# Kernel tuning notes

Measured on AMD Instinct MI355X. Metric: run time of the kernel, lower is better.

The kernel has to match this reference:

```python
import jax, jax.numpy as jnp
import numpy as np

B, T, D = 8, 1024, 1024

def setup_inputs() -> dict:
    key = jax.random.key(0)
    ks = jax.random.split(key, 9)
    s = D ** -0.5
    return {
        "x": jax.random.normal(ks[0], (B, T, D), dtype=jnp.float32),
        "w_q": jax.random.normal(ks[1], (D, D), dtype=jnp.float32) * s,
        "b_q": jax.random.normal(ks[2], (D,), dtype=jnp.float32) * 0.02,
        "w_k": jax.random.normal(ks[3], (D, D), dtype=jnp.float32) * s,
        "b_k": jax.random.normal(ks[4], (D,), dtype=jnp.float32) * 0.02,
        "w_v": jax.random.normal(ks[5], (D, D), dtype=jnp.float32) * s,
        "b_v": jax.random.normal(ks[6], (D,), dtype=jnp.float32) * 0.02,
        "w_o": jax.random.normal(ks[7], (D, D), dtype=jnp.float32) * s,
        "b_o": jax.random.normal(ks[8], (D,), dtype=jnp.float32) * 0.02,
    }

def reference(x, w_q, b_q, w_k, b_k, w_v, b_v, w_o, b_o):
    d = x.shape[-1]
    scale = jnp.asarray(d, x.dtype) ** -0.5
    q = jnp.einsum('btd,ed->bte', x, w_q) + b_q  # nn.Linear: x @ W^T + b
    k = jnp.einsum('btd,ed->bte', x, w_k) + b_k
    v = jnp.einsum('btd,ed->bte', x, w_v) + b_v
    t = x.shape[1]
    causal = jnp.tril(jnp.ones((t, t), dtype=bool))  # (T, T)
    scores = jnp.einsum('bqd,bkd->bqk', q, k) * scale
    scores = jnp.where(causal, scores, -jnp.inf)
    attn = jax.nn.softmax(scores, axis=-1)  # max-subtraction folded in
    out = jnp.einsum('bqk,bkd->bqd', attn, v)
    return jnp.einsum('btd,ed->bte', out, w_o) + b_o
```

## Files before the change

### kernel.cpp

```cpp
#include <hip/hip_runtime.h>

typedef unsigned short u16;
typedef __attribute__((ext_vector_type(8))) short short8;
typedef __attribute__((ext_vector_type(4))) float f32x4;


__device__ __forceinline__ u16 f2bf(float f) {
  unsigned u = __builtin_bit_cast(unsigned, f);
  u += 0x7fffu + ((u >> 16) & 1u);
  return (u16)(u >> 16);
}

__device__ __forceinline__ void gload16(const void* g, void* l) {
  __builtin_amdgcn_global_load_lds(
      (const __attribute__((address_space(1))) unsigned*)g,
      (__attribute__((address_space(3))) unsigned*)l, 16, 0, 0);
}

__device__ __forceinline__ void gemm_tile(
    const u16* __restrict__ A, int lda,
    const u16* __restrict__ B, int ldb,
    int m0, int n0, int kend,
    char* sA, char* sB, f32x4 acc[4][4])
{
  const int tid  = threadIdx.x;
  const int lane = tid & 63;
  const int wave = tid >> 6;
  const int quad = lane >> 4;
  const int l16  = lane & 15;
  const int wr   = (wave >> 1) << 6;
  const int wc   = (wave & 1) << 6;

  const u16* ga[4]; const u16* gb[4]; int lb[4];
#pragma unroll
  for (int j = 0; j < 4; ++j) {
    const int Lb = j * 256 + wave * 64;
    const int L  = Lb + lane;
    const int r  = L >> 3;
    const int c  = (L & 7) ^ (r & 7);
    lb[j] = Lb * 16;
    ga[j] = A + (size_t)(m0 + r) * lda + c * 8;
    gb[j] = B + (size_t)(n0 + r) * ldb + c * 8;
  }

  for (int kt = 0; kt < kend; kt += 64) {
#pragma unroll
    for (int j = 0; j < 4; ++j) {
      gload16(ga[j], sA + lb[j]);
      gload16(gb[j], sB + lb[j]);
      ga[j] += 64; gb[j] += 64;
    }
    __syncthreads();
#pragma unroll
    for (int kk = 0; kk < 2; ++kk) {
      short8 af[4], bfr[4];
#pragma unroll
      for (int i = 0; i < 4; ++i) {
        const int rm = wr + i * 16 + l16;
        af[i]  = *(const short8*)(sA + rm * 128 + (((kk << 2) + quad) ^ (rm & 7)) * 16);
        const int rn = wc + i * 16 + l16;
        bfr[i] = *(const short8*)(sB + rn * 128 + (((kk << 2) + quad) ^ (rn & 7)) * 16);
      }
#pragma unroll
      for (int i = 0; i < 4; ++i)
#pragma unroll
        for (int j = 0; j < 4; ++j)
          acc[i][j] = __builtin_amdgcn_mfma_f32_16x16x32_bf16(af[i], bfr[j], acc[i][j], 0, 0, 0);
    }
    __syncthreads();
  }
}

__device__ __forceinline__ void gemm_tile_64(
    const u16* __restrict__ A, int lda,
    const u16* __restrict__ B, int ldb,
    int m0, int n0, int kend,
    char* sA, char* sB, f32x4 acc[2][4])
{
  const int tid  = threadIdx.x;
  const int lane = tid & 63;
  const int wave = tid >> 6;
  const int quad = lane >> 4;
  const int l16  = lane & 15;
  const int wr   = (wave >> 1) << 5;
  const int wc   = (wave & 1) << 6;

  const u16* ga[2]; int la[2];
  const u16* gb[4]; int lb[4];
#pragma unroll
  for (int j = 0; j < 2; ++j) {
    const int Lb = j * 256 + wave * 64;
    const int L  = Lb + lane;
    const int r  = L >> 3;
    const int c  = (L & 7) ^ (r & 7);
    la[j] = Lb * 16;
    ga[j] = A + (size_t)(m0 + r) * lda + c * 8;
  }
#pragma unroll
  for (int j = 0; j < 4; ++j) {
    const int Lb = j * 256 + wave * 64;
    const int L  = Lb + lane;
    const int r  = L >> 3;
    const int c  = (L & 7) ^ (r & 7);
    lb[j] = Lb * 16;
    gb[j] = B + (size_t)(n0 + r) * ldb + c * 8;
  }

  for (int kt = 0; kt < kend; kt += 64) {
#pragma unroll
    for (int j = 0; j < 2; ++j) { gload16(ga[j], sA + la[j]); ga[j] += 64; }
#pragma unroll
    for (int j = 0; j < 4; ++j) { gload16(gb[j], sB + lb[j]); gb[j] += 64; }
    __syncthreads();
#pragma unroll
    for (int kk = 0; kk < 2; ++kk) {
      short8 af[2], bfr[4];
#pragma unroll
      for (int i = 0; i < 2; ++i) {
        const int rm = wr + i * 16 + l16;
        af[i] = *(const short8*)(sA + rm * 128 + (((kk << 2) + quad) ^ (rm & 7)) * 16);
      }
#pragma unroll
      for (int j = 0; j < 4; ++j) {
        const int rn = wc + j * 16 + l16;
        bfr[j] = *(const short8*)(sB + rn * 128 + (((kk << 2) + quad) ^ (rn & 7)) * 16);
      }
#pragma unroll
      for (int i = 0; i < 2; ++i)
#pragma unroll
        for (int j = 0; j < 4; ++j)
          acc[i][j] = __builtin_amdgcn_mfma_f32_16x16x32_bf16(af[i], bfr[j], acc[i][j], 0, 0, 0);
    }
    __syncthreads();
  }
}

#define ACC_ZERO4(acc) { _Pragma("unroll") for (int i=0;i<4;++i) \
  _Pragma("unroll") for (int j=0;j<4;++j) \
  _Pragma("unroll") for (int r=0;r<4;++r) acc[i][j][r]=0.f; }
#define ACC_ZERO2(acc) { _Pragma("unroll") for (int i=0;i<2;++i) \
  _Pragma("unroll") for (int j=0;j<4;++j) \
  _Pragma("unroll") for (int r=0;r<4;++r) acc[i][j][r]=0.f; }

__device__ __forceinline__ void store_tile_bf16(
    f32x4 acc[4][4], const float* bias, int nbias0,
    u16* C, int m0, int n0, int ldc, char* smem)
{
  const int tid = threadIdx.x, lane = tid & 63, wave = tid >> 6;
  const int quad = lane >> 4, l16 = lane & 15;
  const int wr = (wave >> 1) << 6, wc = (wave & 1) << 6;
  u16* t = (u16*)smem;
#pragma unroll
  for (int j = 0; j < 4; ++j) {
    const int nn = wc + j * 16 + l16;
    const float bj = bias ? bias[nbias0 + nn] : 0.f;
#pragma unroll
    for (int i = 0; i < 4; ++i) {
      const int mm = wr + i * 16 + quad * 4;
#pragma unroll
      for (int r = 0; r < 4; ++r)
        t[(mm + r) * 136 + nn] = f2bf(acc[i][j][r] + bj);
    }
  }
  __syncthreads();
#pragma unroll
  for (int it = 0; it < 8; ++it) {
    const int L = it * 256 + tid;
    const int mm = L >> 4, cc = L & 15;
    *(uint4*)(C + (size_t)(m0 + mm) * ldc + n0 + cc * 8) =
        *(const uint4*)(t + mm * 136 + cc * 8);
  }
}

__global__ __launch_bounds__(256) void cast_inputs(
    const float* __restrict__ x,  const float* __restrict__ wq,
    const float* __restrict__ wk, const float* __restrict__ wv,
    const float* __restrict__ wo,
    u16* xb, u16* wqb, u16* wkb, u16* wvb, u16* wob, float* rsum)
{
  int b = blockIdx.x;
  if (b < 8) {
    float4 z = {0.f, 0.f, 0.f, 0.f};
    *(float4*)(rsum + (b * 256 + threadIdx.x) * 4) = z;
  }
  const float* src; u16* dst; int base;
  if (b < 4096) { src = x; dst = xb; base = b * 2048; }
  else {
    int r = (b - 4096) >> 9, bb = (b - 4096) & 511;
    base = bb * 2048;
    src = (r == 0) ? wq : (r == 1) ? wk : (r == 2) ? wv : wo;
    dst = (r == 0) ? wqb : (r == 1) ? wkb : (r == 2) ? wvb : wob;
  }
  int i0 = base + threadIdx.x * 8;
  float4 f0 = *(const float4*)(src + i0);
  float4 f1 = *(const float4*)(src + i0 + 4);
  short8 o;
  o[0]=(short)f2bf(f0.x); o[1]=(short)f2bf(f0.y); o[2]=(short)f2bf(f0.z); o[3]=(short)f2bf(f0.w);
  o[4]=(short)f2bf(f1.x); o[5]=(short)f2bf(f1.y); o[6]=(short)f2bf(f1.z); o[7]=(short)f2bf(f1.w);
  *(short8*)(dst + i0) = o;
}

__global__ __launch_bounds__(256) void proj_qkv(
    const u16* __restrict__ xb,
    const u16* __restrict__ wqb, const u16* __restrict__ wkb, const u16* __restrict__ wvb,
    const float* __restrict__ bq, const float* __restrict__ bk, const float* __restrict__ bv,
    u16* q, u16* k, u16* vt)
{
  __shared__ char smem[34816];
  char* sA = smem; char* sB = smem + 16384;
  const int z = blockIdx.z;
  const u16* W = (z == 0) ? wqb : (z == 1) ? wkb : wvb;
  const float* bias = (z == 0) ? bq : (z == 1) ? bk : bv;
  const int id = blockIdx.x + 8 * blockIdx.y;
  const int m0 = ((id & 7) * 8 + (id >> 6)) * 128;
  const int n0 = ((id >> 3) & 7) * 128;

  f32x4 acc[4][4]; ACC_ZERO4(acc);
  gemm_tile(xb, 1024, W, 1024, m0, n0, 1024, sA, sB, acc);

  if (z < 2) {
    store_tile_bf16(acc, bias, n0, (z == 0) ? q : k, m0, n0, 1024, smem);
  } else {
    const int tid = threadIdx.x, lane = tid & 63, wave = tid >> 6;
    const int quad = lane >> 4, l16 = lane & 15;
    const int wr = (wave >> 1) << 6, wc = (wave & 1) << 6;
    u16* t = (u16*)smem;
#pragma unroll
    for (int j = 0; j < 4; ++j) {
      const int nn = wc + j * 16 + l16;
      const float bj = bias[n0 + nn];
#pragma unroll
      for (int i = 0; i < 4; ++i) {
        const int mm = wr + i * 16 + quad * 4;
#pragma unroll
        for (int r = 0; r < 4; ++r)
          t[nn * 136 + mm + r] = f2bf(acc[i][j][r] + bj);
      }
    }
    __syncthreads();
    const int b = m0 >> 10, t0 = m0 & 1023;
#pragma unroll
    for (int it = 0; it < 8; ++it) {
      const int L = it * 256 + tid;
      const int nn = L >> 4, cc = L & 15;
      *(uint4*)(vt + ((size_t)b << 20) + (size_t)(n0 + nn) * 1024 + t0 + cc * 8) =
          *(const uint4*)(t + nn * 136 + cc * 8);
    }
  }
}

__global__ __launch_bounds__(256) void qk_expscores(
    const u16* __restrict__ q, const u16* __restrict__ k,
    u16* __restrict__ probs, float* __restrict__ rowsum)
{
  const int id = blockIdx.x;
  const int b = id / 72, t = id - b * 72;
  int p = (int)((__builtin_sqrtf((float)(4 * t + 1)) - 1.f) * 0.5f);
  while ((p + 1) * (p + 2) <= t) ++p;
  while (p * (p + 1) > t) --p;
  int r0 = t - p * (p + 1);
  const int qi = 2 * p + (r0 >= p + 1);
  const int kb = (r0 >= p + 1) ? r0 - (p + 1) : r0;

  __shared__ char smem[24576];
  char* sA = smem; char* sB = smem + 8192;
  const u16* A = q + ((size_t)b << 20);
  const u16* B = k + ((size_t)b << 20);
  const int m0 = qi * 64, n0 = kb * 128;

  f32x4 acc[2][4]; ACC_ZERO2(acc);
  gemm_tile_64(A, 1024, B, 1024, m0, n0, 1024, sA, sB, acc);

  const int tid = threadIdx.x, lane = tid & 63, wave = tid >> 6;
  const int quad = lane >> 4, l16 = lane & 15;
  const int wr = (wave >> 1) << 5, wc = (wave & 1) << 6;
  const bool diag = (kb == (qi >> 1));

  float part[2][4];
#pragma unroll
  for (int i = 0; i < 2; ++i)
#pragma unroll
    for (int r = 0; r < 4; ++r) part[i][r] = 0.f;

  u16* tl = (u16*)smem;
#pragma unroll
  for (int j = 0; j < 4; ++j) {
    const int nn = wc + j * 16 + l16;
#pragma unroll
    for (int i = 0; i < 2; ++i) {
      const int mm = wr + i * 16 + quad * 4;
#pragma unroll
      for (int r = 0; r < 4; ++r) {
        float e = __expf(acc[i][j][r] * 0.03125f);
        if (diag && (n0 + nn) > (m0 + mm + r)) e = 0.f;
        part[i][r] += e;
        tl[(mm + r) * 136 + nn] = f2bf(e);
      }
    }
  }
  float* rs = rowsum + b * 1024 + m0;
#pragma unroll
  for (int i = 0; i < 2; ++i)
#pragma unroll
    for (int r = 0; r < 4; ++r) {
      float v = part[i][r];
      v += __shfl_xor(v, 1); v += __shfl_xor(v, 2);
      v += __shfl_xor(v, 4); v += __shfl_xor(v, 8);
      if (l16 == 0) atomicAdd(rs + wr + i * 16 + quad * 4 + r, v);
    }
  __syncthreads();
  u16* C = probs + ((size_t)b << 20);
#pragma unroll
  for (int it = 0; it < 4; ++it) {
    const int L = it * 256 + tid;
    const int mm = L >> 4, cc = L & 15;
    *(uint4*)(C + (size_t)(m0 + mm) * 1024 + n0 + cc * 8) =
        *(const uint4*)(tl + mm * 136 + cc * 8);
  }
}

__global__ __launch_bounds__(256) void pv_gemm(
    const u16* __restrict__ probs, const u16* __restrict__ vt,
    const float* __restrict__ rowsum, u16* __restrict__ o)
{
  const int id = blockIdx.x;
  const int b = id & 7, nb = (id >> 3) & 7, qi = 15 - (id >> 6);
  __shared__ char smem[24576];
  char* sA = smem; char* sB = smem + 8192;
  const u16* A = probs + ((size_t)b << 20);
  const u16* B = vt + ((size_t)b << 20);
  const int m0 = qi * 64, n0 = nb * 128;
  const int kend = (qi + 1) * 64;

  f32x4 acc[2][4]; ACC_ZERO2(acc);
  gemm_tile_64(A, 1024, B, 1024, m0, n0, kend, sA, sB, acc);

  const int tid = threadIdx.x, lane = tid & 63, wave = tid >> 6;
  const int quad = lane >> 4, l16 = lane & 15;
  const int wr = (wave >> 1) << 5, wc = (wave & 1) << 6;
  const float* rs = rowsum + b * 1024 + m0;
  u16* tl = (u16*)smem;
#pragma unroll
  for (int i = 0; i < 2; ++i)
#pragma unroll
    for (int r = 0; r < 4; ++r) {
      const int mm = wr + i * 16 + quad * 4 + r;
      const float inv = 1.0f / rs[mm];
#pragma unroll
      for (int j = 0; j < 4; ++j)
        tl[mm * 136 + wc + j * 16 + l16] = f2bf(acc[i][j][r] * inv);
    }
  __syncthreads();
  u16* C = o + ((size_t)b << 20);
#pragma unroll
  for (int it = 0; it < 4; ++it) {
    const int L = it * 256 + tid;
    const int mm = L >> 4, cc = L & 15;
    *(uint4*)(C + (size_t)(m0 + mm) * 1024 + n0 + cc * 8) =
        *(const uint4*)(tl + mm * 136 + cc * 8);
  }
}

__global__ __launch_bounds__(256) void proj_o(
    const u16* __restrict__ ob, const u16* __restrict__ wob,
    const float* __restrict__ bo, float* __restrict__ out)
{
  __shared__ char smem[34816];
  char* sA = smem; char* sB = smem + 8192;
  const int id = blockIdx.x;
  const int m0 = ((id & 7) * 16 + (id >> 6)) * 64;
  const int n0 = ((id >> 3) & 7) * 128;
  f32x4 acc[2][4]; ACC_ZERO2(acc);
  gemm_tile_64(ob, 1024, wob, 1024, m0, n0, 1024, sA, sB, acc);

  const int tid = threadIdx.x, lane = tid & 63, wave = tid >> 6;
  const int quad = lane >> 4, l16 = lane & 15;
  const int wr = (wave >> 1) << 5, wc = (wave & 1) << 6;
  float* tf = (float*)smem;
#pragma unroll
  for (int j = 0; j < 4; ++j) {
    const int nn = wc + j * 16 + l16;
    const float bj = bo[n0 + nn];
#pragma unroll
    for (int i = 0; i < 2; ++i)
#pragma unroll
      for (int r = 0; r < 4; ++r)
        tf[(wr + i * 16 + quad * 4 + r) * 132 + nn] = acc[i][j][r] + bj;
  }
  __syncthreads();
#pragma unroll
  for (int it = 0; it < 8; ++it) {
    const int L = it * 256 + tid;
    const int mm = L >> 5, cc = L & 31;
    *(float4*)(out + (size_t)(m0 + mm) * 1024 + n0 + cc * 4) =
        *(const float4*)(tf + mm * 132 + cc * 4);
  }
}

extern "C" void kernel_launch(void* const* d_in, const int* in_sizes, int n_in,
                              void* d_out, int out_size, void* d_ws, size_t ws_size,
                              hipStream_t stream) {
  const float* x  = (const float*)d_in[0];
  const float* wq = (const float*)d_in[1];
  const float* bq = (const float*)d_in[2];
  const float* wk = (const float*)d_in[3];
  const float* bk = (const float*)d_in[4];
  const float* wv = (const float*)d_in[5];
  const float* bv = (const float*)d_in[6];
  const float* wo = (const float*)d_in[7];
  const float* bo = (const float*)d_in[8];
  float* out = (float*)d_out;

  char* ws = (char*)d_ws;
  const size_t MB = 1u << 20;
  u16*  xb  = (u16*)(ws);
  u16*  wqb = (u16*)(ws + 16*MB);
  u16*  wkb = (u16*)(ws + 18*MB);
  u16*  wvb = (u16*)(ws + 20*MB);
  u16*  wob = (u16*)(ws + 22*MB);
  u16*  qb  = (u16*)(ws + 24*MB);
  u16*  kb  = (u16*)(ws + 40*MB);
  u16*  vtb = (u16*)(ws + 56*MB);
  u16*  pr  = (u16*)(ws + 72*MB);
  float* rsum = (float*)(ws + 88*MB);

  cast_inputs<<<6144, 256, 0, stream>>>(x, wq, wk, wv, wo, xb, wqb, wkb, wvb, wob, rsum);
  proj_qkv<<<dim3(8, 64, 3), 256, 0, stream>>>(xb, wqb, wkb, wvb, bq, bk, bv, qb, kb, vtb);
  qk_expscores<<<576, 256, 0, stream>>>(qb, kb, pr, rsum);
  pv_gemm<<<1024, 256, 0, stream>>>(pr, vtb, rsum, xb );
  proj_o<<<1024, 256, 0, stream>>>(xb, wob, bo, out);
}
```

Measured before the change: 225.8 us.

## Fuse Q and K projections to share the X tile across two weight tiles

Splits the combined QKV projection into a fused Q+K kernel and a separate V kernel. The Q+K kernel loads each X tile into LDS once and multiplies it against both the W_q and W_k tiles, keeping two 64-float accumulator sets per thread. This removes one of the redundant X tile loads and halves the X traffic for Q and K. In exchange it doubles accumulator register pressure (lower occupancy), uses more LDS, and adds a second kernel launch for V.

```diff
diff --git a/kernel.cpp b/kernel.cpp
--- a/kernel.cpp
+++ b/kernel.cpp
@@ -200,52 +200,112 @@
   *(short8*)(dst + i0) = o;
 }
 
-__global__ __launch_bounds__(256) void proj_qkv(
+__global__ __launch_bounds__(256) void proj_qk(
     const u16* __restrict__ xb,
-    const u16* __restrict__ wqb, const u16* __restrict__ wkb, const u16* __restrict__ wvb,
-    const float* __restrict__ bq, const float* __restrict__ bk, const float* __restrict__ bv,
-    u16* q, u16* k, u16* vt)
+    const u16* __restrict__ wqb, const u16* __restrict__ wkb,
+    const float* __restrict__ bq, const float* __restrict__ bk,
+    u16* q, u16* k)
+{
+  __shared__ char smem[49152];
+  char* sA = smem; char* sQ = smem + 16384; char* sK = smem + 32768;
+  const int id = blockIdx.x;
+  const int m0 = ((id & 7) * 8 + (id >> 6)) * 128;
+  const int n0 = ((id >> 3) & 7) * 128;
+
+  const int tid = threadIdx.x, lane = tid & 63, wave = tid >> 6;
+  const int quad = lane >> 4, l16 = lane & 15;
+  const int wr = (wave >> 1) << 6, wc = (wave & 1) << 6;
+
+  const u16* ga[4]; const u16* gq[4]; const u16* gk[4]; int lb[4];
+#pragma unroll
+  for (int j = 0; j < 4; ++j) {
+    const int Lb = j * 256 + wave * 64;
+    const int L  = Lb + lane;
+    const int r  = L >> 3;
+    const int c  = (L & 7) ^ (r & 7);
+    lb[j] = Lb * 16;
+    ga[j] = xb  + (size_t)(m0 + r) * 1024 + c * 8;
+    gq[j] = wqb + (size_t)(n0 + r) * 1024 + c * 8;
+    gk[j] = wkb + (size_t)(n0 + r) * 1024 + c * 8;
+  }
+
+  f32x4 accQ[4][4], accK[4][4];
+  ACC_ZERO4(accQ); ACC_ZERO4(accK);
+
+  for (int kt = 0; kt < 1024; kt += 64) {
+#pragma unroll
+    for (int j = 0; j < 4; ++j) {
+      gload16(ga[j], sA + lb[j]);
+      gload16(gq[j], sQ + lb[j]);
+      gload16(gk[j], sK + lb[j]);
+      ga[j] += 64; gq[j] += 64; gk[j] += 64;
+    }
+    __syncthreads();
+#pragma unroll
+    for (int kk = 0; kk < 2; ++kk) {
+      short8 af[4], bqf[4], bkf[4];
+#pragma unroll
+      for (int i = 0; i < 4; ++i) {
+        const int rm = wr + i * 16 + l16;
+        const int rn = wc + i * 16 + l16;
+        const int co = (kk << 2) + quad;
+        af[i]  = *(const short8*)(sA + rm * 128 + ((co ^ (rm & 7)) * 16));
+        bqf[i] = *(const short8*)(sQ + rn * 128 + ((co ^ (rn & 7)) * 16));
+        bkf[i] = *(const short8*)(sK + rn * 128 + ((co ^ (rn & 7)) * 16));
+      }
+#pragma unroll
+      for (int i = 0; i < 4; ++i)
+#pragma unroll
+        for (int j = 0; j < 4; ++j) {
+          accQ[i][j] = __builtin_amdgcn_mfma_f32_16x16x32_bf16(af[i], bqf[j], accQ[i][j], 0, 0, 0);
+          accK[i][j] = __builtin_amdgcn_mfma_f32_16x16x32_bf16(af[i], bkf[j], accK[i][j], 0, 0, 0);
+        }
+    }
+    __syncthreads();
+  }
+
+  store_tile_bf16(accQ, bq, n0, q, m0, n0, 1024, smem);
+  __syncthreads();
+  store_tile_bf16(accK, bk, n0, k, m0, n0, 1024, smem);
+}
+
+__global__ __launch_bounds__(256) void proj_v(
+    const u16* __restrict__ xb, const u16* __restrict__ wvb,
+    const float* __restrict__ bv, u16* vt)
 {
   __shared__ char smem[34816];
   char* sA = smem; char* sB = smem + 16384;
-  const int z = blockIdx.z;
-  const u16* W = (z == 0) ? wqb : (z == 1) ? wkb : wvb;
-  const float* bias = (z == 0) ? bq : (z == 1) ? bk : bv;
-  const int id = blockIdx.x + 8 * blockIdx.y;
+  const int id = blockIdx.x;
   const int m0 = ((id & 7) * 8 + (id >> 6)) * 128;
   const int n0 = ((id >> 3) & 7) * 128;
 
   f32x4 acc[4][4]; ACC_ZERO4(acc);
-  gemm_tile(xb, 1024, W, 1024, m0, n0, 1024, sA, sB, acc);
-
-  if (z < 2) {
-    store_tile_bf16(acc, bias, n0, (z == 0) ? q : k, m0, n0, 1024, smem);
-  } else {
-    const int tid = threadIdx.x, lane = tid & 63, wave = tid >> 6;
-    const int quad = lane >> 4, l16 = lane & 15;
-    const int wr = (wave >> 1) << 6, wc = (wave & 1) << 6;
-    u16* t = (u16*)smem;
-#pragma unroll
-    for (int j = 0; j < 4; ++j) {
-      const int nn = wc + j * 16 + l16;
-      const float bj = bias[n0 + nn];
-#pragma unroll
-      for (int i = 0; i < 4; ++i) {
-        const int mm = wr + i * 16 + quad * 4;
-#pragma unroll
-        for (int r = 0; r < 4; ++r)
-          t[nn * 136 + mm + r] = f2bf(acc[i][j][r] + bj);
-      }
-    }
-    __syncthreads();
-    const int b = m0 >> 10, t0 = m0 & 1023;
-#pragma unroll
-    for (int it = 0; it < 8; ++it) {
-      const int L = it * 256 + tid;
-      const int nn = L >> 4, cc = L & 15;
-      *(uint4*)(vt + ((size_t)b << 20) + (size_t)(n0 + nn) * 1024 + t0 + cc * 8) =
-          *(const uint4*)(t + nn * 136 + cc * 8);
-    }
+  gemm_tile(xb, 1024, wvb, 1024, m0, n0, 1024, sA, sB, acc);
+
+  const int tid = threadIdx.x, lane = tid & 63, wave = tid >> 6;
+  const int quad = lane >> 4, l16 = lane & 15;
+  const int wr = (wave >> 1) << 6, wc = (wave & 1) << 6;
+  u16* t = (u16*)smem;
+#pragma unroll
+  for (int j = 0; j < 4; ++j) {
+    const int nn = wc + j * 16 + l16;
+    const float bj = bv[n0 + nn];
+#pragma unroll
+    for (int i = 0; i < 4; ++i) {
+      const int mm = wr + i * 16 + quad * 4;
+#pragma unroll
+      for (int r = 0; r < 4; ++r)
+        t[nn * 136 + mm + r] = f2bf(acc[i][j][r] + bj);
+    }
+  }
+  __syncthreads();
+  const int b = m0 >> 10, t0 = m0 & 1023;
+#pragma unroll
+  for (int it = 0; it < 8; ++it) {
+    const int L = it * 256 + tid;
+    const int nn = L >> 4, cc = L & 15;
+    *(uint4*)(vt + ((size_t)b << 20) + (size_t)(n0 + nn) * 1024 + t0 + cc * 8) =
+        *(const uint4*)(t + nn * 136 + cc * 8);
   }
 }
 
@@ -425,7 +485,8 @@
   float* rsum = (float*)(ws + 88*MB);
 
   cast_inputs<<<6144, 256, 0, stream>>>(x, wq, wk, wv, wo, xb, wqb, wkb, wvb, wob, rsum);
-  proj_qkv<<<dim3(8, 64, 3), 256, 0, stream>>>(xb, wqb, wkb, wvb, bq, bk, bv, qb, kb, vtb);
+  proj_qk<<<512, 256, 0, stream>>>(xb, wqb, wkb, bq, bk, qb, kb);
+  proj_v<<<512, 256, 0, stream>>>(xb, wvb, bv, vtb);
   qk_expscores<<<576, 256, 0, stream>>>(qb, kb, pr, rsum);
   pv_gemm<<<1024, 256, 0, stream>>>(pr, vtb, rsum, xb );
   proj_o<<<1024, 256, 0, stream>>>(xb, wob, bo, out);
```

Result: slower. 250.6 us (+11.0%).
